# Optimization experiments

Hardware: AMD Instinct MI355X
Metric: run time of the kernel (lower is better)

## Reference

```python
import jax, jax.numpy as jnp
import numpy as np

EMPTY_IDX = 6  # relabeling of the original -1 ('EMPTY') expert to row 6 of the stacked tables


def setup_inputs() -> dict:
    key = jax.random.key(0)
    k1, k2, k3, k4, k5, k6 = jax.random.split(key, 6)
    B, L, H, T, E = 32, 2048, 768, 12, 7
    return {
        "sequence_output": jax.random.normal(k1, (B, L, H), dtype=jnp.float32),
        "module_net_w": jax.random.normal(k2, (E, H, H), dtype=jnp.float32),
        "span_net_w": jax.random.normal(k3, (E, H, 2), dtype=jnp.float32),
        "turns": jax.random.randint(k4, (B, T, 2), 0, L),
        "key_phrase_span": jax.random.randint(k5, (B, T, 2), 0, L),
        "module_index": jax.random.randint(k6, (B, T), 0, E),
    }


def reference(sequence_output, module_net_w, span_net_w, turns, key_phrase_span, module_index):
    seq = sequence_output            # [B, L, H]
    B, L, H = seq.shape
    T = turns.shape[1]
    f32 = seq.dtype

    eidx = module_index              # [B, T], 0..6 (6 == EMPTY, original -1)
    mod_mask = (eidx != EMPTY_IDX).astype(f32)            # module_index != -1
    start_pos = turns[:, :, 0]       # [B, T] turn start token positions
    turns_mask = (start_pos >= 0).astype(f32)             # turns[:,:,0] != -1

    # context_hidden_step = sequence_output[arange(B), start] for every step
    ctx = jnp.take_along_axis(seq, start_pos[:, :, None], axis=1)   # [B, T, H]

    # einsum('bh,bhz,blz->blz'): (ctx @ W_expert) broadcast-multiplied with seq.
    # Compute ctx @ W for ALL experts (tables are tiny), then gather per (b, t).
    cW_all = jnp.einsum('bth,ehz->btez', ctx, module_net_w)         # [B, T, 7, H]
    gidx = jnp.broadcast_to(eidx[:, :, None, None], (B, T, 1, H))
    cW = jnp.take_along_axis(cW_all, gidx, axis=2).squeeze(2)       # [B, T, H]

    span_w = span_net_w[eidx]        # [B, T, H, 2] per-sample expert span weights
    # logits[b,t,l,k] = sum_z seq[b,l,z] * cW[b,t,z] * span_w[b,t,z,k]
    v = cW[..., None] * span_w                                      # [B, T, H, 2]
    logits = jnp.einsum('blz,btzk->btlk', seq, v)                   # [B, T, L, 2]

    # CrossEntropyLoss(ignore_index=-1, reduction='none') over the L axis
    logsm = jax.nn.log_softmax(logits, axis=2)                      # [B, T, L, 2]
    tgt = key_phrase_span[:, :, :T][:, :T]  # [B, T, 2]
    tgt = key_phrase_span
    safe = jnp.clip(tgt, 0, L - 1)                                  # [B, T, 2]
    picked = jnp.take_along_axis(logsm, safe[:, :, None, :], axis=2).squeeze(2)  # [B, T, 2]
    ce = jnp.where(tgt >= 0, -picked, jnp.zeros((), f32))           # [B, T, 2]
    step_loss = 0.5 * (ce[..., 0] + ce[..., 1]) * mod_mask          # [B, T]

    loss = (step_loss * turns_mask).sum() / turns_mask.sum()
    return loss
```

## Files before the change

### kernel.cpp

```cpp
#include <hip/hip_runtime.h>
#include <math.h>

#define Bz 32
#define Lz 2048
#define Hz 768
#define Tz 12
#define Ez 7
#define EMPTYIDX 6
#define NCOL 24
#define NITEM (Bz * Tz)
#define LCHUNK 64
#define NCHUNK 32

__global__ void k0_compact(const int* __restrict__ midx,
                           int* __restrict__ off, int* __restrict__ items) {
    __shared__ int cnt[Ez];
    __shared__ int offs[Ez + 1];
    int tid = threadIdx.x;
    if (tid < Ez) cnt[tid] = 0;
    __syncthreads();
    int e = midx[tid];
    e = min(max(e, 0), Ez - 1);
    int r = atomicAdd(&cnt[e], 1);
    __syncthreads();
    if (tid == 0) {
        int acc = 0;
        for (int j = 0; j < Ez; ++j) { offs[j] = acc; acc += cnt[j]; }
        offs[Ez] = acc;
    }
    __syncthreads();
    items[offs[e] + r] = tid;
    if (tid <= Ez) off[tid] = offs[tid];
}

#define K1A_ZC 3
#define K1A_HB 48
#define K1A_HC 16
__global__ void k1a_cw(const float* __restrict__ seq, const float* __restrict__ W,
                       const int* __restrict__ turns,
                       const int* __restrict__ off, const int* __restrict__ items,
                       float* __restrict__ pc) {
    int bx = blockIdx.x;
    int e  = bx % Ez;
    int zc = (bx / Ez) % K1A_ZC;
    int hc = bx / (Ez * K1A_ZC);
    int z  = zc * 256 + threadIdx.x;
    int h0 = hc * K1A_HB;
    int off0 = off[e];
    int cnt  = off[e + 1] - off0;
    const float* Wb = W + ((size_t)e * Hz + h0) * Hz + z;
    float w[K1A_HB];
#pragma unroll
    for (int j = 0; j < K1A_HB; ++j) w[j] = Wb[(size_t)j * Hz];

    for (int n = 0; n < cnt; ++n) {
        int i  = items[off0 + n];
        int b  = i / Tz;
        int st = turns[2 * i];
        st = min(max(st, 0), Lz - 1);
        const float* c = seq + ((size_t)(b * Lz + st)) * Hz + h0;
        float acc = 0.f;
#pragma unroll
        for (int j = 0; j < K1A_HB; ++j) acc = fmaf(c[j], w[j], acc);
        pc[((size_t)hc * NITEM + i) * Hz + z] = acc;
    }
}

__global__ void k1b_v(const float* __restrict__ pc, const float* __restrict__ spanw,
                      const int* __restrict__ midx, float* __restrict__ v) {
    int idx = blockIdx.x * 256 + threadIdx.x;
    int i = idx / Hz;
    int z = idx - i * Hz;
    float cw = 0.f;
#pragma unroll
    for (int hc = 0; hc < K1A_HC; ++hc)
        cw += pc[((size_t)hc * NITEM + i) * Hz + z];
    int e = midx[i];
    e = min(max(e, 0), Ez - 1);
    int b = i / Tz, t = i - b * Tz;
    size_t vb = ((size_t)(b * NCOL + t * 2)) * Hz + z;
    v[vb]      = cw * spanw[(e * Hz + z) * 2 + 0];
    v[vb + Hz] = cw * spanw[(e * Hz + z) * 2 + 1];
}

#define BKP 64
#define NPH (Hz / BKP)

typedef float4 F4;

__device__ __forceinline__ float dot16(const float* __restrict__ vp,
                                       F4 a0, F4 a1, F4 a2, F4 a3) {
    const F4* vq = (const F4*)vp;
    F4 q0 = vq[0], q1 = vq[1], q2 = vq[2], q3 = vq[3];
    float s0 = 0.f, s1 = 0.f, s2 = 0.f, s3 = 0.f;
    s0 = fmaf(a0.x, q0.x, s0); s1 = fmaf(a0.y, q0.y, s1);
    s2 = fmaf(a0.z, q0.z, s2); s3 = fmaf(a0.w, q0.w, s3);
    s0 = fmaf(a1.x, q1.x, s0); s1 = fmaf(a1.y, q1.y, s1);
    s2 = fmaf(a1.z, q1.z, s2); s3 = fmaf(a1.w, q1.w, s3);
    s0 = fmaf(a2.x, q2.x, s0); s1 = fmaf(a2.y, q2.y, s1);
    s2 = fmaf(a2.z, q2.z, s2); s3 = fmaf(a2.w, q2.w, s3);
    s0 = fmaf(a3.x, q3.x, s0); s1 = fmaf(a3.y, q3.y, s1);
    s2 = fmaf(a3.z, q3.z, s2); s3 = fmaf(a3.w, q3.w, s3);
    return (s0 + s1) + (s2 + s3);
}

#define C_LIST(X) X(0) X(1) X(2) X(3) X(4) X(5) X(6) X(7) X(8) X(9) X(10) X(11) \
                  X(12) X(13) X(14) X(15) X(16) X(17) X(18) X(19) X(20) X(21) X(22) X(23)

__global__ __launch_bounds__(256, 4)
void k2_logits(const float* __restrict__ seq, const float* __restrict__ v,
               const int* __restrict__ kps,
               float* __restrict__ pm, float* __restrict__ ps,
               float* __restrict__ picked) {
    int bx  = blockIdx.x;
    int b   = bx / NCHUNK;
    int ch  = bx % NCHUNK;
    int l0  = ch * LCHUNK;
    int tid = threadIdx.x;
    int r   = tid & (LCHUNK - 1);
    int kq  = __builtin_amdgcn_readfirstlane(tid >> 6);

    __shared__ float at[LCHUNK][BKP];
    __shared__ float bufA[LCHUNK][NCOL + 1];
    __shared__ float bufB[LCHUNK][NCOL + 1];
    __shared__ float bufC[LCHUNK][NCOL + 1];
    __shared__ float redm[NCOL][4], reds[NCOL][4];
    __shared__ int   ksafe[NCOL];

    if (tid < NCOL) {
        int t0 = kps[b * NCOL + tid];
        ksafe[tid] = min(max(t0, 0), Lz - 1);
    }

#define DECL_ACC(n) float c##n = 0.f;
    C_LIST(DECL_ACC)
#undef DECL_ACC

    const float* A = seq + ((size_t)b * Lz + l0) * Hz;
    const float* V = v + (size_t)b * NCOL * Hz;

    int rb   = tid >> 4;
    int cq   = tid & 15;
    int slot = ((cq ^ rb) << 2);
    const float* Ab0 = A + (size_t)rb * Hz + (cq << 2);
    float* Sb = &at[0][0] + rb * BKP + slot;

    int rx = r & 15;
    const float* arow = &at[r][0];
    const float* ap0 = arow + (((kq * 4 + 0) ^ rx) << 2);
    const float* ap1 = arow + (((kq * 4 + 1) ^ rx) << 2);
    const float* ap2 = arow + (((kq * 4 + 2) ^ rx) << 2);
    const float* ap3 = arow + (((kq * 4 + 3) ^ rx) << 2);

    F4 g0, g1, g2, g3;
#define LOADG(KOFF) do { const float* Ap_ = Ab0 + (KOFF);            \
        g0 = *(const F4*)&Ap_[0 * 16 * Hz];                          \
        g1 = *(const F4*)&Ap_[1 * 16 * Hz];                          \
        g2 = *(const F4*)&Ap_[2 * 16 * Hz];                          \
        g3 = *(const F4*)&Ap_[3 * 16 * Hz]; } while (0)

    LOADG(0);

#pragma unroll 1
    for (int ph = 0; ph < NPH; ++ph) {
        __syncthreads();
        *(F4*)&Sb[0 * 1024] = g0;  *(F4*)&Sb[1 * 1024] = g1;
        *(F4*)&Sb[2 * 1024] = g2;  *(F4*)&Sb[3 * 1024] = g3;
        __syncthreads();
        if (ph + 1 < NPH) LOADG((ph + 1) * BKP);

        F4 a0 = *(const F4*)ap0, a1 = *(const F4*)ap1,
           a2 = *(const F4*)ap2, a3 = *(const F4*)ap3;

        const float* Vp = V + ph * BKP + kq * 16;
#define DO_COL(n) c##n += dot16(Vp + (n) * Hz, a0, a1, a2, a3);
        C_LIST(DO_COL)
#undef DO_COL
    }
#undef LOADG

    __syncthreads();
    if (kq == 1) {
#define ST_A(n) bufA[r][n] = c##n;
        C_LIST(ST_A)
#undef ST_A
    } else if (kq == 2) {
#define ST_B(n) bufB[r][n] = c##n;
        C_LIST(ST_B)
#undef ST_B
    } else if (kq == 3) {
#define ST_C(n) bufC[r][n] = c##n;
        C_LIST(ST_C)
#undef ST_C
    }
    __syncthreads();
    if (kq == 0) {
        int grow = l0 + r;
#define MG(n) { c##n += bufA[r][n] + bufB[r][n] + bufC[r][n]; bufA[r][n] = c##n; \
                if (ksafe[n] == grow) picked[b * NCOL + (n)] = c##n; }
        C_LIST(MG)
#undef MG
    }
    __syncthreads();

    if (tid < 96) {
        int c = tid >> 2, rg = tid & 3;
        float m = bufA[rg * 16][c];
        for (int rr = rg * 16 + 1; rr < rg * 16 + 16; ++rr)
            m = fmaxf(m, bufA[rr][c]);
        float s = 0.f;
        for (int rr = rg * 16; rr < rg * 16 + 16; ++rr)
            s += expf(bufA[rr][c] - m);
        redm[c][rg] = m; reds[c][rg] = s;
    }
    __syncthreads();
    if (tid < NCOL) {
        float m = redm[tid][0];
        for (int j = 1; j < 4; ++j) m = fmaxf(m, redm[tid][j]);
        float s = 0.f;
        for (int j = 0; j < 4; ++j) s += reds[tid][j] * expf(redm[tid][j] - m);
        pm[((size_t)b * NCOL + tid) * NCHUNK + ch] = m;
        ps[((size_t)b * NCOL + tid) * NCHUNK + ch] = s;
    }
}

__global__ void k4_final(const int* __restrict__ midx, const int* __restrict__ turns,
                         const int* __restrict__ kps,
                         const float* __restrict__ pm, const float* __restrict__ ps,
                         const float* __restrict__ picked, float* __restrict__ out) {
    int tid = threadIdx.x;
    int i = tid;
    int b = i / Tz, t = i % Tz;
    int e = midx[i];
    float modm  = (e != EMPTYIDX) ? 1.f : 0.f;
    float tmask = (turns[2 * i] >= 0) ? 1.f : 0.f;
    float ce[2];
#pragma unroll
    for (int k = 0; k < 2; ++k) {
        int c = t * 2 + k;
        const float* pmr = pm + ((size_t)b * NCOL + c) * NCHUNK;
        const float* psr = ps + ((size_t)b * NCOL + c) * NCHUNK;
        float m = pmr[0];
        for (int chn = 1; chn < NCHUNK; ++chn) m = fmaxf(m, pmr[chn]);
        float s = 0.f;
        for (int chn = 0; chn < NCHUNK; ++chn) s += psr[chn] * expf(pmr[chn] - m);
        float lse = m + logf(s);
        int tgt = kps[2 * i + k];
        ce[k] = (tgt >= 0) ? (lse - picked[b * NCOL + c]) : 0.f;
    }
    float contrib = 0.5f * (ce[0] + ce[1]) * modm * tmask;

    __shared__ float wsum[6], wmask[6];
    float sl = contrib, sm = tmask;
    for (int o = 32; o > 0; o >>= 1) {
        sl += __shfl_down(sl, o, 64);
        sm += __shfl_down(sm, o, 64);
    }
    int w = tid >> 6, lane = tid & 63;
    if (lane == 0) { wsum[w] = sl; wmask[w] = sm; }
    __syncthreads();
    if (tid == 0) {
        float a = 0.f, mk = 0.f;
        for (int ww = 0; ww < 6; ++ww) { a += wsum[ww]; mk += wmask[ww]; }
        out[0] = a / mk;
    }
}

extern "C" void kernel_launch(void* const* d_in, const int* in_sizes, int n_in,
                              void* d_out, int out_size, void* d_ws, size_t ws_size,
                              hipStream_t stream) {
    const float* seq   = (const float*)d_in[0];
    const float* W     = (const float*)d_in[1];
    const float* spanw = (const float*)d_in[2];
    const int*   turns = (const int*)d_in[3];
    const int*   kps   = (const int*)d_in[4];
    const int*   midx  = (const int*)d_in[5];
    float* out = (float*)d_out;

    char* ws = (char*)d_ws;
    int*   off    = (int*)(ws + 0);
    int*   items  = (int*)(ws + 256);
    float* pc     = (float*)(ws + 2048);
    float* v      = (float*)(ws + 2048 + 18874368);
    float* pm     = (float*)(ws + 2048 + 18874368 + 2359296);
    float* ps     = (float*)(ws + 2048 + 18874368 + 2359296 + 98304);
    float* picked = (float*)(ws + 2048 + 18874368 + 2359296 + 196608);

    hipLaunchKernelGGL(k0_compact, dim3(1), dim3(NITEM), 0, stream, midx, off, items);
    hipLaunchKernelGGL(k1a_cw, dim3(Ez * K1A_ZC * K1A_HC), dim3(256), 0, stream,
                       seq, W, turns, off, items, pc);
    hipLaunchKernelGGL(k1b_v, dim3((NITEM * Hz) / 256), dim3(256), 0, stream,
                       pc, spanw, midx, v);
    hipLaunchKernelGGL(k2_logits, dim3(Bz * NCHUNK), dim3(256), 0, stream,
                       seq, v, kps, pm, ps, picked);
    hipLaunchKernelGGL(k4_final, dim3(1), dim3(NITEM), 0, stream,
                       midx, turns, kps, pm, ps, picked, out);
}
```

Measured before the change: 379.5 us.

## Remap logits threads to two rows each with k-split reduced by shuffles

In the logits kernel, threads now split into 32 row-pairs times 8 k-slices. Each thread holds two row accumulators per column, so each vector load of v feeds both rows and global/L1 traffic on v per FMA is halved. The cross-thread k reduction now uses wave shuffles instead of three shared-memory staging buffers, which cuts LDS use and one barrier phase. The cost is doubled accumulator registers (48 instead of 24) and more shuffle instructions, which may pressure occupancy at launch_bounds(256,4).

```diff
diff --git a/kernel.cpp b/kernel.cpp
--- a/kernel.cpp
+++ b/kernel.cpp
@@ -88,22 +88,6 @@
 
 typedef float4 F4;
 
-__device__ __forceinline__ float dot16(const float* __restrict__ vp,
-                                       F4 a0, F4 a1, F4 a2, F4 a3) {
-    const F4* vq = (const F4*)vp;
-    F4 q0 = vq[0], q1 = vq[1], q2 = vq[2], q3 = vq[3];
-    float s0 = 0.f, s1 = 0.f, s2 = 0.f, s3 = 0.f;
-    s0 = fmaf(a0.x, q0.x, s0); s1 = fmaf(a0.y, q0.y, s1);
-    s2 = fmaf(a0.z, q0.z, s2); s3 = fmaf(a0.w, q0.w, s3);
-    s0 = fmaf(a1.x, q1.x, s0); s1 = fmaf(a1.y, q1.y, s1);
-    s2 = fmaf(a1.z, q1.z, s2); s3 = fmaf(a1.w, q1.w, s3);
-    s0 = fmaf(a2.x, q2.x, s0); s1 = fmaf(a2.y, q2.y, s1);
-    s2 = fmaf(a2.z, q2.z, s2); s3 = fmaf(a2.w, q2.w, s3);
-    s0 = fmaf(a3.x, q3.x, s0); s1 = fmaf(a3.y, q3.y, s1);
-    s2 = fmaf(a3.z, q3.z, s2); s3 = fmaf(a3.w, q3.w, s3);
-    return (s0 + s1) + (s2 + s3);
-}
-
 #define C_LIST(X) X(0) X(1) X(2) X(3) X(4) X(5) X(6) X(7) X(8) X(9) X(10) X(11) \
                   X(12) X(13) X(14) X(15) X(16) X(17) X(18) X(19) X(20) X(21) X(22) X(23)
 
@@ -117,13 +101,11 @@
     int ch  = bx % NCHUNK;
     int l0  = ch * LCHUNK;
     int tid = threadIdx.x;
-    int r   = tid & (LCHUNK - 1);
-    int kq  = __builtin_amdgcn_readfirstlane(tid >> 6);
+    int rp  = tid >> 3;
+    int kq  = tid & 7;
 
     __shared__ float at[LCHUNK][BKP];
-    __shared__ float bufA[LCHUNK][NCOL + 1];
-    __shared__ float bufB[LCHUNK][NCOL + 1];
-    __shared__ float bufC[LCHUNK][NCOL + 1];
+    __shared__ float lgbuf[LCHUNK][NCOL + 1];
     __shared__ float redm[NCOL][4], reds[NCOL][4];
     __shared__ int   ksafe[NCOL];
 
@@ -132,7 +114,7 @@
         ksafe[tid] = min(max(t0, 0), Lz - 1);
     }
 
-#define DECL_ACC(n) float c##n = 0.f;
+#define DECL_ACC(n) float cA##n = 0.f; float cB##n = 0.f;
     C_LIST(DECL_ACC)
 #undef DECL_ACC
 
@@ -145,12 +127,13 @@
     const float* Ab0 = A + (size_t)rb * Hz + (cq << 2);
     float* Sb = &at[0][0] + rb * BKP + slot;
 
-    int rx = r & 15;
-    const float* arow = &at[r][0];
-    const float* ap0 = arow + (((kq * 4 + 0) ^ rx) << 2);
-    const float* ap1 = arow + (((kq * 4 + 1) ^ rx) << 2);
-    const float* ap2 = arow + (((kq * 4 + 2) ^ rx) << 2);
-    const float* ap3 = arow + (((kq * 4 + 3) ^ rx) << 2);
+    int rx = rp & 15;
+    const float* rowA = &at[rp][0];
+    const float* rowB = &at[rp + 32][0];
+    int s0 = (((2 * kq + 0) ^ rx) << 2);
+    int s1 = (((2 * kq + 1) ^ rx) << 2);
+    const float* apA0 = rowA + s0;  const float* apA1 = rowA + s1;
+    const float* apB0 = rowB + s0;  const float* apB1 = rowB + s1;
 
     F4 g0, g1, g2, g3;
 #define LOADG(KOFF) do { const float* Ap_ = Ab0 + (KOFF);            \
@@ -169,35 +152,38 @@
         __syncthreads();
         if (ph + 1 < NPH) LOADG((ph + 1) * BKP);
 
-        F4 a0 = *(const F4*)ap0, a1 = *(const F4*)ap1,
-           a2 = *(const F4*)ap2, a3 = *(const F4*)ap3;
-
-        const float* Vp = V + ph * BKP + kq * 16;
-#define DO_COL(n) c##n += dot16(Vp + (n) * Hz, a0, a1, a2, a3);
+        F4 aA0 = *(const F4*)apA0, aA1 = *(const F4*)apA1;
+        F4 aB0 = *(const F4*)apB0, aB1 = *(const F4*)apB1;
+
+        const float* Vp = V + ph * BKP + kq * 8;
+#define DO_COL(n) { const F4* vq_ = (const F4*)(Vp + (n) * Hz);       \
+        F4 v0_ = vq_[0], v1_ = vq_[1];                                \
+        cA##n = fmaf(aA0.x, v0_.x, cA##n); cA##n = fmaf(aA0.y, v0_.y, cA##n); \
+        cA##n = fmaf(aA0.z, v0_.z, cA##n); cA##n = fmaf(aA0.w, v0_.w, cA##n); \
+        cA##n = fmaf(aA1.x, v1_.x, cA##n); cA##n = fmaf(aA1.y, v1_.y, cA##n); \
+        cA##n = fmaf(aA1.z, v1_.z, cA##n); cA##n = fmaf(aA1.w, v1_.w, cA##n); \
+        cB##n = fmaf(aB0.x, v0_.x, cB##n); cB##n = fmaf(aB0.y, v0_.y, cB##n); \
+        cB##n = fmaf(aB0.z, v0_.z, cB##n); cB##n = fmaf(aB0.w, v0_.w, cB##n); \
+        cB##n = fmaf(aB1.x, v1_.x, cB##n); cB##n = fmaf(aB1.y, v1_.y, cB##n); \
+        cB##n = fmaf(aB1.z, v1_.z, cB##n); cB##n = fmaf(aB1.w, v1_.w, cB##n); }
         C_LIST(DO_COL)
 #undef DO_COL
     }
 #undef LOADG
 
-    __syncthreads();
-    if (kq == 1) {
-#define ST_A(n) bufA[r][n] = c##n;
-        C_LIST(ST_A)
-#undef ST_A
-    } else if (kq == 2) {
-#define ST_B(n) bufB[r][n] = c##n;
-        C_LIST(ST_B)
-#undef ST_B
-    } else if (kq == 3) {
-#define ST_C(n) bufC[r][n] = c##n;
-        C_LIST(ST_C)
-#undef ST_C
-    }
+#define RED(n) { cA##n += __shfl_xor(cA##n, 1); cA##n += __shfl_xor(cA##n, 2); \
+                 cA##n += __shfl_xor(cA##n, 4);                                \
+                 cB##n += __shfl_xor(cB##n, 1); cB##n += __shfl_xor(cB##n, 2); \
+                 cB##n += __shfl_xor(cB##n, 4); }
+    C_LIST(RED)
+#undef RED
+
     __syncthreads();
     if (kq == 0) {
-        int grow = l0 + r;
-#define MG(n) { c##n += bufA[r][n] + bufB[r][n] + bufC[r][n]; bufA[r][n] = c##n; \
-                if (ksafe[n] == grow) picked[b * NCOL + (n)] = c##n; }
+        int g0r = l0 + rp, g1r = l0 + rp + 32;
+#define MG(n) { lgbuf[rp][n] = cA##n; lgbuf[rp + 32][n] = cB##n;               \
+                if (ksafe[n] == g0r) picked[b * NCOL + (n)] = cA##n;           \
+                if (ksafe[n] == g1r) picked[b * NCOL + (n)] = cB##n; }
         C_LIST(MG)
 #undef MG
     }
@@ -205,12 +191,12 @@
 
     if (tid < 96) {
         int c = tid >> 2, rg = tid & 3;
-        float m = bufA[rg * 16][c];
+        float m = lgbuf[rg * 16][c];
         for (int rr = rg * 16 + 1; rr < rg * 16 + 16; ++rr)
-            m = fmaxf(m, bufA[rr][c]);
+            m = fmaxf(m, lgbuf[rr][c]);
         float s = 0.f;
         for (int rr = rg * 16; rr < rg * 16 + 16; ++rr)
-            s += expf(bufA[rr][c] - m);
+            s += expf(lgbuf[rr][c] - m);
         redm[c][rg] = m; reds[c][rg] = s;
     }
     __syncthreads();
```

New measurement: 426.0 us. 12.3% more time.
